# Performance work log

Measured on AMD Instinct MI355X. Metric: run time of the kernel, lower is better.

## Reference

```python
import jax, jax.numpy as jnp
import numpy as np

K = 2048      # codebook_size
D = 64        # codebook_dim
B = 32
T = 4096
W = 0.99      # codebook_loss_weight (EMA decay)
THRESH = 1.0  # discard_vec_threshold


def setup_inputs() -> dict:
    key = jax.random.key(0)
    k1, k2 = jax.random.split(key, 2)
    x = jax.random.normal(k1, (B, D, T), jnp.float32)
    codebook = jax.random.normal(k2, (K, D), jnp.float32)
    codebook_avg = codebook.copy()
    vector_usage = jnp.ones((K,), jnp.float32)
    perm = jnp.arange(B * T, dtype=jnp.int32)  # deterministic stand-in for randperm
    return dict(x=x, codebook=codebook, codebook_avg=codebook_avg,
                vector_usage=vector_usage, perm=perm)


def reference(x, codebook, codebook_avg, vector_usage, perm):
    Bv, E, Tv = x.shape
    sg = jax.lax.stop_gradient
    # preprocess: [B, E, T] -> [N, E]
    xf = jnp.transpose(x, (0, 2, 1)).reshape(-1, E)
    N = xf.shape[0]
    x_norm = jnp.linalg.norm(xf - jnp.mean(xf)) / np.sqrt(N * E)
    # squared euclidean distances [N, K]
    d = (jnp.sum(xf * xf, axis=-1, keepdims=True)
         - 2.0 * (xf @ codebook.T)
         + jnp.sum(codebook * codebook, axis=-1))
    idx = jnp.argmin(d, axis=-1)            # [N]
    fit = jnp.mean(jnp.min(d, axis=-1))
    q = codebook[idx]                       # [N, E] gather
    # --- update_codebook (torch.no_grad) ---
    cb_sum = jax.ops.segment_sum(sg(xf), idx, num_segments=K)          # onehot @ x
    counts = jax.ops.segment_sum(jnp.ones((N,), xf.dtype), idx, num_segments=K)
    new_avg = W * sg(codebook_avg) + (1.0 - W) * cb_sum
    new_usage = W * sg(vector_usage) + (1.0 - W) * counts
    keep = (new_usage >= THRESH).astype(xf.dtype)[:, None]
    random_shift = sg(xf)[perm][:K]
    new_codebook = keep * (new_avg / new_usage[:, None]) + (1.0 - keep) * random_shift
    vector_prob = counts / jnp.sum(counts)
    entropy = -jnp.sum(vector_prob * jnp.log(vector_prob + 1e-8))
    codebook_diff = jnp.linalg.norm(new_codebook - sg(codebook)) / np.sqrt(K * E)
    # --- commitment loss + straight-through ---
    commit_loss = jnp.sum((sg(q) - xf) ** 2) / (N * E)
    out = xf + sg(q - xf)
    out = jnp.transpose(out.reshape(Bv, Tv, E), (0, 2, 1))  # [B, E, T]
    return (out, commit_loss, fit, x_norm, new_codebook, new_avg, new_usage,
            entropy, codebook_diff)
```

## Files before the change

kernel.cpp:

```cpp
#include <hip/hip_runtime.h>
#include <math.h>

#define OUT_X      0
#define OUT_COMMIT 8388608
#define OUT_FIT    8388609
#define OUT_XNORM  8388610
#define OUT_NCB    8388611
#define OUT_NAVG   (8388611 + 131072)
#define OUT_NUSE   (8388611 + 262144)
#define OUT_ENT    (8388611 + 264192)
#define OUT_CBDIFF (8388611 + 264193)

#define WS_DACC    0
#define WS_COUNTS  64
#define WS_CBSUM   8256
#define WS_CURS    532544
#define WS_XN2     540736
#define WS_IDX     1065024
#define WS_CN2H    1589312
#define WS_SORTED  1597504
#define WS_CHI     2121792
#define WS_CLO     2383936
#define WS_ZERO_BYTES 532544

#define LO_SCALE5  32.0f

typedef _Float16 f16x8_t __attribute__((ext_vector_type(8)));
typedef float f32x16_t __attribute__((ext_vector_type(16)));

__device__ __forceinline__ void gload_lds16(const _Float16* g, _Float16* l) {
    __builtin_amdgcn_global_load_lds(
        (const __attribute__((address_space(1))) unsigned int*)(g),
        (__attribute__((address_space(3))) unsigned int*)(l), 16, 0, 0);
}

__global__ __launch_bounds__(256) void kern_prep_x(
    const float* __restrict__ x, float* __restrict__ xt,
    float* __restrict__ xn2, double* __restrict__ dacc)
{
    __shared__ __align__(16) float Xs[64][128];
    __shared__ float tmpA[4], tmpB[4];
    const int tid = threadIdx.x;
    const int n0 = blockIdx.x * 128;
    const int b = n0 >> 12, t0 = n0 & 4095;
    const float* xb = x + ((size_t)b << 18) + t0;
#pragma unroll
    for (int i = 0; i < 8; ++i) {
        int c = i * 256 + tid;
        int e = c >> 5, v4 = c & 31;
        float4 f = *(const float4*)(xb + ((size_t)e << 12) + (v4 << 2));
        *(float4*)&Xs[e][v4 << 2] = f;
    }
    __syncthreads();
    const int q = tid & 3, r0 = tid >> 2;
    float s1t = 0.f, s2t = 0.f;
#pragma unroll
    for (int h = 0; h < 2; ++h) {
        int r = r0 + (h << 6);
        float s2 = 0.f;
#pragma unroll
        for (int j = 0; j < 4; ++j) {
            int e = q * 16 + j * 4;
            float4 f = make_float4(Xs[e][r], Xs[e + 1][r], Xs[e + 2][r], Xs[e + 3][r]);
            *(float4*)(xt + (((size_t)(n0 + r)) << 6) + e) = f;
            s1t += f.x + f.y + f.z + f.w;
            s2 += f.x * f.x + f.y * f.y + f.z * f.z + f.w * f.w;
        }
        s2t += s2;
        float s2q = s2 + __shfl_xor(s2, 1, 64);
        s2q += __shfl_xor(s2q, 2, 64);
        if (q == 0) xn2[n0 + r] = s2q;
    }
    float rs = s1t, r2 = s2t;
#pragma unroll
    for (int m = 32; m >= 1; m >>= 1) {
        rs += __shfl_xor(rs, m, 64);
        r2 += __shfl_xor(r2, m, 64);
    }
    if ((tid & 63) == 0) { tmpA[tid >> 6] = rs; tmpB[tid >> 6] = r2; }
    __syncthreads();
    if (tid == 0) {
        atomicAdd(&dacc[0], (double)(tmpA[0] + tmpA[1] + tmpA[2] + tmpA[3]));
        atomicAdd(&dacc[1], (double)(tmpB[0] + tmpB[1] + tmpB[2] + tmpB[3]));
    }
}

__global__ __launch_bounds__(256) void kern_prep_cb(
    const float* __restrict__ cb, _Float16* __restrict__ chi,
    _Float16* __restrict__ clo, float* __restrict__ cn2h)
{
    __shared__ float Cs[128][68];
    const int tid = threadIdx.x;
    const int c0 = blockIdx.x * 128;
#pragma unroll
    for (int i = 0; i < 8; ++i) {
        int li = i * 256 + tid;
        int code = li >> 4, d4 = li & 15;
        float4 f = *(const float4*)(cb + (((size_t)(c0 + code)) << 6) + (d4 << 2));
        Cs[code][d4 * 4 + 0] = f.x; Cs[code][d4 * 4 + 1] = f.y;
        Cs[code][d4 * 4 + 2] = f.z; Cs[code][d4 * 4 + 3] = f.w;
    }
    __syncthreads();
    const int w = tid >> 6, lane = tid & 63;
    const int cl = (w << 5) + (lane & 31);
    const int g = lane >> 5;
    const int ktg = blockIdx.x * 4 + w;
#pragma unroll
    for (int s = 0; s < 4; ++s) {
        f16x8_t hh, ll;
#pragma unroll
        for (int i = 0; i < 8; ++i) {
            int k = 16 * s + 4 * g + (i & 3) + 8 * (i >> 2);
            float v = Cs[cl][k];
            _Float16 h = (_Float16)v;
            hh[i] = h;
            ll[i] = (_Float16)((v - (float)h) * LO_SCALE5);
        }
        *(f16x8_t*)(chi + (((size_t)(ktg * 4 + s)) << 9) + lane * 8) = hh;
        *(f16x8_t*)(clo + (((size_t)(ktg * 4 + s)) << 9) + lane * 8) = ll;
    }
    if (tid < 128) {
        float s = 0.f;
#pragma unroll
        for (int k = 0; k < 64; ++k) { float v = Cs[tid][k]; s = fmaf(v, v, s); }
        cn2h[c0 + tid] = -0.5f * s;
    }
}

__global__ __launch_bounds__(256, 2) void kern_argmin_mfma(
    const float* __restrict__ xt, const float* __restrict__ cn2h,
    const _Float16* __restrict__ chi, const _Float16* __restrict__ clo,
    const float* __restrict__ xn2, int* __restrict__ idxb,
    unsigned* __restrict__ counts, double* __restrict__ dacc)
{
    __shared__ __align__(16) _Float16 Bs[3][2][8][512];
    __shared__ float cvs[2048];
    const int tid = threadIdx.x;
    const int w = tid >> 6, lane = tid & 63;
    const int n0 = blockIdx.x * 256 + w * 64;
    const int l31 = lane & 31, g = lane >> 5;

    for (int i = tid; i < 2048; i += 256) cvs[i] = cn2h[i];

    f16x8_t ahi[2][4], alo5[2][4];
#pragma unroll
    for (int rb = 0; rb < 2; ++rb) {
        const float* xr = xt + ((size_t)(n0 + rb * 32 + l31) << 6) + 4 * g;
#pragma unroll
        for (int s = 0; s < 4; ++s) {
            float4 p = *(const float4*)(xr + 16 * s);
            float4 q = *(const float4*)(xr + 16 * s + 8);
            float vals[8] = {p.x, p.y, p.z, p.w, q.x, q.y, q.z, q.w};
#pragma unroll
            for (int i = 0; i < 8; ++i) {
                _Float16 h = (_Float16)vals[i];
                ahi[rb][s][i] = h;
                alo5[rb][s][i] = (_Float16)((vals[i] - (float)h) * LO_SCALE5);
            }
        }
    }
    float bestm[2][16]; int besti[2][16];
#pragma unroll
    for (int rb = 0; rb < 2; ++rb)
#pragma unroll
        for (int r = 0; r < 16; ++r) { bestm[rb][r] = -INFINITY; besti[rb][r] = 0; }

    __syncthreads();

#pragma unroll
    for (int kt = 0; kt < 2; ++kt)
#pragma unroll
        for (int j = 0; j < 4; ++j) {
            int seg = (j << 2) | w;
            int tt = seg >> 3, sh = seg & 7;
            const _Float16* src = ((sh & 1) ? clo : chi)
                + ((((size_t)(kt * 2 + tt)) * 4 + (sh >> 1)) << 9) + lane * 8;
            gload_lds16(src, &Bs[kt][tt][sh][0]);
        }

    int cur = 0, nxt = 2;
    for (int kt = 0; kt < 32; ++kt) {
        if (kt < 30) asm volatile("s_waitcnt vmcnt(4)" ::: "memory");
        else         asm volatile("s_waitcnt vmcnt(0)" ::: "memory");
        __builtin_amdgcn_s_barrier();
        if (kt + 2 < 32) {
#pragma unroll
            for (int j = 0; j < 4; ++j) {
                int seg = (j << 2) | w;
                int tt = seg >> 3, sh = seg & 7;
                const _Float16* src = ((sh & 1) ? clo : chi)
                    + ((((size_t)((kt + 2) * 2 + tt)) * 4 + (sh >> 1)) << 9) + lane * 8;
                gload_lds16(src, &Bs[nxt][tt][sh][0]);
            }
        }
#pragma unroll
        for (int tt = 0; tt < 2; ++tt) {
            const int tg = kt * 2 + tt;
            f16x8_t bh[4], bl[4];
#pragma unroll
            for (int s = 0; s < 4; ++s) {
                bh[s] = *(const f16x8_t*)&Bs[cur][tt][s * 2 + 0][lane * 8];
                bl[s] = *(const f16x8_t*)&Bs[cur][tt][s * 2 + 1][lane * 8];
            }
            float cv = cvs[(tg << 5) + l31];
            f32x16_t a0, a1;
#pragma unroll
            for (int r = 0; r < 16; ++r) { a0[r] = cv; a1[r] = cv; }
#pragma unroll
            for (int s = 0; s < 4; ++s) {
                a0 = __builtin_amdgcn_mfma_f32_32x32x16_f16(ahi[0][s], bh[s], a0, 0, 0, 0);
                a1 = __builtin_amdgcn_mfma_f32_32x32x16_f16(ahi[1][s], bh[s], a1, 0, 0, 0);
                f16x8_t bh5 = bh[s] * (_Float16)0.03125f;
                a0 = __builtin_amdgcn_mfma_f32_32x32x16_f16(alo5[0][s], bh5, a0, 0, 0, 0);
                a1 = __builtin_amdgcn_mfma_f32_32x32x16_f16(alo5[1][s], bh5, a1, 0, 0, 0);
                f16x8_t h50 = ahi[0][s] * (_Float16)0.03125f;
                f16x8_t h51 = ahi[1][s] * (_Float16)0.03125f;
                a0 = __builtin_amdgcn_mfma_f32_32x32x16_f16(h50, bl[s], a0, 0, 0, 0);
                a1 = __builtin_amdgcn_mfma_f32_32x32x16_f16(h51, bl[s], a1, 0, 0, 0);
            }
#pragma unroll
            for (int r = 0; r < 16; ++r) {
                if (a0[r] > bestm[0][r]) { bestm[0][r] = a0[r]; besti[0][r] = tg; }
                if (a1[r] > bestm[1][r]) { bestm[1][r] = a1[r]; besti[1][r] = tg; }
            }
        }
        cur = (cur == 2) ? 0 : cur + 1;
        nxt = (nxt == 2) ? 0 : nxt + 1;
    }
    float fs = 0.f;
#pragma unroll
    for (int rb = 0; rb < 2; ++rb)
#pragma unroll
        for (int r = 0; r < 16; ++r) {
            float mv = bestm[rb][r]; int mi = (besti[rb][r] << 5) + l31;
#pragma unroll
            for (int m = 1; m < 32; m <<= 1) {
                float ov = __shfl_xor(mv, m, 64);
                int oi = __shfl_xor(mi, m, 64);
                if (ov > mv || (ov == mv && oi < mi)) { mv = ov; mi = oi; }
            }
            if (l31 == 0) {
                int row = (r & 3) + 8 * (r >> 2) + 4 * g;
                int n = n0 + rb * 32 + row;
                idxb[n] = mi;
                atomicAdd(&counts[mi], 1u);
                fs += xn2[n] - 2.f * mv;
            }
        }
    if (l31 == 0) atomicAdd(&dacc[2], (double)fs);
}

__global__ void kern_scan(const unsigned* __restrict__ counts, unsigned* __restrict__ curs) {
    __shared__ unsigned wtot[4];
    const int tid = threadIdx.x;
    const int base = tid * 8;
    unsigned s[8]; unsigned tot = 0;
#pragma unroll
    for (int j = 0; j < 8; ++j) { s[j] = counts[base + j]; tot += s[j]; }
    unsigned v = tot;
    const int lane = tid & 63;
#pragma unroll
    for (int d = 1; d < 64; d <<= 1) {
        unsigned o = (unsigned)__shfl_up((int)v, d, 64);
        if (lane >= d) v += o;
    }
    if (lane == 63) wtot[tid >> 6] = v;
    __syncthreads();
    unsigned wbase = 0;
    for (int w = 0; w < (tid >> 6); ++w) wbase += wtot[w];
    unsigned run = wbase + v - tot;
#pragma unroll
    for (int j = 0; j < 8; ++j) { curs[base + j] = run; run += s[j]; }
}

__global__ void kern_scatter(const int* __restrict__ idxb, unsigned* __restrict__ curs,
                             unsigned* __restrict__ sorted) {
    const int n = blockIdx.x * 256 + threadIdx.x;
    int k = idxb[n];
    unsigned pos = atomicAdd(&curs[k], 1u);
    sorted[pos] = ((unsigned)k << 17) | (unsigned)n;
}

__global__ __launch_bounds__(256) void kern_chunk_reduce(
    const float* __restrict__ xt, const unsigned* __restrict__ sorted,
    float* __restrict__ cb_sum)
{
    const int tid = threadIdx.x;
    const int w = tid >> 6, lane = tid & 63;
    const int base = blockIdx.x * 256 + w * 64;
    int kcur = (int)(sorted[base] >> 17);
    float acc = 0.f;
#pragma unroll 4
    for (int it = 0; it < 16; ++it) {
        uint4 p = *(const uint4*)&sorted[base + it * 4];
        float v0 = xt[((size_t)(p.x & 0x1FFFFu) << 6) + lane];
        float v1 = xt[((size_t)(p.y & 0x1FFFFu) << 6) + lane];
        float v2 = xt[((size_t)(p.z & 0x1FFFFu) << 6) + lane];
        float v3 = xt[((size_t)(p.w & 0x1FFFFu) << 6) + lane];
        int k0 = (int)(p.x >> 17), k1 = (int)(p.y >> 17);
        int k2 = (int)(p.z >> 17), k3 = (int)(p.w >> 17);
        if (k0 != kcur) { atomicAdd(&cb_sum[(kcur << 6) + lane], acc); kcur = k0; acc = 0.f; }
        acc += v0;
        if (k1 != kcur) { atomicAdd(&cb_sum[(kcur << 6) + lane], acc); kcur = k1; acc = 0.f; }
        acc += v1;
        if (k2 != kcur) { atomicAdd(&cb_sum[(kcur << 6) + lane], acc); kcur = k2; acc = 0.f; }
        acc += v2;
        if (k3 != kcur) { atomicAdd(&cb_sum[(kcur << 6) + lane], acc); kcur = k3; acc = 0.f; }
        acc += v3;
    }
    atomicAdd(&cb_sum[(kcur << 6) + lane], acc);
}

__global__ __launch_bounds__(256) void kern_update(
    const float* __restrict__ cb_sum, const unsigned* __restrict__ counts,
    const float* __restrict__ cb, const float* __restrict__ cba,
    const float* __restrict__ usage, const int* __restrict__ perm,
    const float* __restrict__ xt, float* __restrict__ out,
    double* __restrict__ dacc)
{
    const int tid = threadIdx.x;
    const int i = blockIdx.x * 256 + tid;
    const int k = i >> 6, e = i & 63;
    float na = 0.99f * cba[i] + 0.01f * cb_sum[i];
    float nu = 0.99f * usage[k] + 0.01f * (float)counts[k];
    float ncb = (nu >= 1.0f) ? (na / nu)
                             : xt[((size_t)perm[k] << 6) + e];
    out[OUT_NAVG + i] = na;
    out[OUT_NCB + i] = ncb;
    if (e == 0) out[OUT_NUSE + k] = nu;
    float d = ncb - cb[i];
    float dd = d * d;
#pragma unroll
    for (int m = 32; m >= 1; m >>= 1) dd += __shfl_xor(dd, m, 64);
    if (e == 0) atomicAdd(&dacc[4], (double)dd);
}

__global__ __launch_bounds__(256) void kern_out(
    const float* __restrict__ x, const float* __restrict__ cb,
    const int* __restrict__ idxb, float* __restrict__ out,
    double* __restrict__ dacc) {
    __shared__ float tmp[4];
    const int tid = threadIdx.x;
    const int n0 = blockIdx.x * 256 + (tid & 63) * 4;
    const int ec = tid >> 6;
    const int b = n0 >> 12, t = n0 & 4095;
    int4 k4 = *(const int4*)(idxb + n0);
    const float* xb = x + ((size_t)b << 18) + t;
    float* ob = out + OUT_X + ((size_t)b << 18) + t;
    float cl = 0.f;
#pragma unroll
    for (int j = 0; j < 16; ++j) {
        int e = ec * 16 + j;
        float4 xv = *(const float4*)(xb + ((size_t)e << 12));
        float q0 = cb[((size_t)k4.x << 6) + e], q1 = cb[((size_t)k4.y << 6) + e];
        float q2 = cb[((size_t)k4.z << 6) + e], q3 = cb[((size_t)k4.w << 6) + e];
        float r0 = q0 - xv.x, r1 = q1 - xv.y, r2 = q2 - xv.z, r3 = q3 - xv.w;
        cl += r0 * r0 + r1 * r1 + r2 * r2 + r3 * r3;
        *(float4*)(ob + ((size_t)e << 12)) = make_float4(q0, q1, q2, q3);
    }
#pragma unroll
    for (int m = 32; m >= 1; m >>= 1) cl += __shfl_xor(cl, m, 64);
    if ((tid & 63) == 0) tmp[tid >> 6] = cl;
    __syncthreads();
    if (tid == 0) atomicAdd(&dacc[3], (double)(tmp[0] + tmp[1] + tmp[2] + tmp[3]));
}

__global__ void kern_scalars(const unsigned* __restrict__ counts,
                             const double* __restrict__ dacc, float* __restrict__ out) {
    __shared__ float tmp[4];
    __shared__ float totalSh;
    const int tid = threadIdx.x;
    float c = 0.f;
    for (int k = tid; k < 2048; k += 256) c += (float)counts[k];
#pragma unroll
    for (int m = 32; m >= 1; m >>= 1) c += __shfl_xor(c, m, 64);
    if ((tid & 63) == 0) tmp[tid >> 6] = c;
    __syncthreads();
    if (tid == 0) totalSh = tmp[0] + tmp[1] + tmp[2] + tmp[3];
    __syncthreads();
    const float total = totalSh;
    float ent = 0.f;
    for (int k = tid; k < 2048; k += 256) {
        float p = (float)counts[k] / total;
        ent -= p * logf(p + 1e-8f);
    }
#pragma unroll
    for (int m = 32; m >= 1; m >>= 1) ent += __shfl_xor(ent, m, 64);
    __syncthreads();
    if ((tid & 63) == 0) tmp[tid >> 6] = ent;
    __syncthreads();
    if (tid == 0) {
        float entropy = tmp[0] + tmp[1] + tmp[2] + tmp[3];
        out[OUT_COMMIT] = (float)(dacc[3] / 8388608.0);
        out[OUT_FIT]    = (float)(dacc[2] / 131072.0);
        double nd = 8388608.0;
        double var = dacc[1] - dacc[0] * dacc[0] / nd;
        if (var < 0.0) var = 0.0;
        out[OUT_XNORM] = (float)(sqrt(var) / sqrt(nd));
        out[OUT_ENT] = entropy;
        out[OUT_CBDIFF] = (float)(sqrt(dacc[4]) / sqrt(131072.0));
    }
}

extern "C" void kernel_launch(void* const* d_in, const int* in_sizes, int n_in,
                              void* d_out, int out_size, void* d_ws, size_t ws_size,
                              hipStream_t stream) {
    const float* x     = (const float*)d_in[0];
    const float* cb    = (const float*)d_in[1];
    const float* cba   = (const float*)d_in[2];
    const float* usage = (const float*)d_in[3];
    const int*   perm  = (const int*)d_in[4];
    float* out = (float*)d_out;
    char* ws = (char*)d_ws;
    double*    dacc   = (double*)(ws + WS_DACC);
    unsigned*  counts = (unsigned*)(ws + WS_COUNTS);
    float*     cbsum  = (float*)(ws + WS_CBSUM);
    unsigned*  curs   = (unsigned*)(ws + WS_CURS);
    float*     xn2    = (float*)(ws + WS_XN2);
    int*       idxb   = (int*)(ws + WS_IDX);
    float*     cn2h   = (float*)(ws + WS_CN2H);
    unsigned*  sorted = (unsigned*)(ws + WS_SORTED);
    _Float16*  chi    = (_Float16*)(ws + WS_CHI);
    _Float16*  clo    = (_Float16*)(ws + WS_CLO);
    float*     xt     = out + OUT_X;

    hipMemsetAsync(ws, 0, WS_ZERO_BYTES, stream);
    kern_prep_x<<<1024, 256, 0, stream>>>(x, xt, xn2, dacc);
    kern_prep_cb<<<16, 256, 0, stream>>>(cb, chi, clo, cn2h);
    kern_argmin_mfma<<<512, 256, 0, stream>>>(xt, cn2h, chi, clo, xn2, idxb, counts, dacc);
    kern_scan<<<1, 256, 0, stream>>>(counts, curs);
    kern_scatter<<<512, 256, 0, stream>>>(idxb, curs, sorted);
    kern_chunk_reduce<<<512, 256, 0, stream>>>(xt, sorted, cbsum);
    kern_update<<<512, 256, 0, stream>>>(cbsum, counts, cb, cba, usage, perm, xt, out, dacc);
    kern_out<<<512, 256, 0, stream>>>(x, cb, idxb, out, dacc);
    kern_scalars<<<1, 256, 0, stream>>>(counts, dacc, out);
}
```

Before: 276.4 us.

## Split codebook across blocks with atomicMax merge, fuse prep kernels, derive commit from fit

```diff
diff --git a/kernel.cpp b/kernel.cpp
--- a/kernel.cpp
+++ b/kernel.cpp
@@ -14,14 +14,15 @@
 #define WS_DACC    0
 #define WS_COUNTS  64
 #define WS_CBSUM   8256
-#define WS_CURS    532544
-#define WS_XN2     540736
-#define WS_IDX     1065024
-#define WS_CN2H    1589312
-#define WS_SORTED  1597504
-#define WS_CHI     2121792
-#define WS_CLO     2383936
-#define WS_ZERO_BYTES 532544
+#define WS_BEST    532544
+#define WS_CURS    1581120
+#define WS_XN2     1589312
+#define WS_IDX     2113600
+#define WS_CN2H    2637888
+#define WS_SORTED  2646080
+#define WS_CHI     3170368
+#define WS_CLO     3432512
+#define WS_ZERO_BYTES 1581120
 
 #define LO_SCALE5  32.0f
 
@@ -34,220 +35,232 @@
         (__attribute__((address_space(3))) unsigned int*)(l), 16, 0, 0);
 }
 
-__global__ __launch_bounds__(256) void kern_prep_x(
+__global__ __launch_bounds__(256) void kern_prep(
     const float* __restrict__ x, float* __restrict__ xt,
-    float* __restrict__ xn2, double* __restrict__ dacc)
-{
-    __shared__ __align__(16) float Xs[64][128];
-    __shared__ float tmpA[4], tmpB[4];
-    const int tid = threadIdx.x;
-    const int n0 = blockIdx.x * 128;
-    const int b = n0 >> 12, t0 = n0 & 4095;
-    const float* xb = x + ((size_t)b << 18) + t0;
-#pragma unroll
-    for (int i = 0; i < 8; ++i) {
-        int c = i * 256 + tid;
-        int e = c >> 5, v4 = c & 31;
-        float4 f = *(const float4*)(xb + ((size_t)e << 12) + (v4 << 2));
-        *(float4*)&Xs[e][v4 << 2] = f;
-    }
-    __syncthreads();
-    const int q = tid & 3, r0 = tid >> 2;
-    float s1t = 0.f, s2t = 0.f;
-#pragma unroll
-    for (int h = 0; h < 2; ++h) {
-        int r = r0 + (h << 6);
-        float s2 = 0.f;
-#pragma unroll
-        for (int j = 0; j < 4; ++j) {
-            int e = q * 16 + j * 4;
-            float4 f = make_float4(Xs[e][r], Xs[e + 1][r], Xs[e + 2][r], Xs[e + 3][r]);
-            *(float4*)(xt + (((size_t)(n0 + r)) << 6) + e) = f;
-            s1t += f.x + f.y + f.z + f.w;
-            s2 += f.x * f.x + f.y * f.y + f.z * f.z + f.w * f.w;
-        }
-        s2t += s2;
-        float s2q = s2 + __shfl_xor(s2, 1, 64);
-        s2q += __shfl_xor(s2q, 2, 64);
-        if (q == 0) xn2[n0 + r] = s2q;
-    }
-    float rs = s1t, r2 = s2t;
-#pragma unroll
-    for (int m = 32; m >= 1; m >>= 1) {
-        rs += __shfl_xor(rs, m, 64);
-        r2 += __shfl_xor(r2, m, 64);
-    }
-    if ((tid & 63) == 0) { tmpA[tid >> 6] = rs; tmpB[tid >> 6] = r2; }
-    __syncthreads();
-    if (tid == 0) {
-        atomicAdd(&dacc[0], (double)(tmpA[0] + tmpA[1] + tmpA[2] + tmpA[3]));
-        atomicAdd(&dacc[1], (double)(tmpB[0] + tmpB[1] + tmpB[2] + tmpB[3]));
-    }
-}
-
-__global__ __launch_bounds__(256) void kern_prep_cb(
+    float* __restrict__ xn2, double* __restrict__ dacc,
     const float* __restrict__ cb, _Float16* __restrict__ chi,
     _Float16* __restrict__ clo, float* __restrict__ cn2h)
 {
-    __shared__ float Cs[128][68];
-    const int tid = threadIdx.x;
-    const int c0 = blockIdx.x * 128;
-#pragma unroll
-    for (int i = 0; i < 8; ++i) {
-        int li = i * 256 + tid;
-        int code = li >> 4, d4 = li & 15;
-        float4 f = *(const float4*)(cb + (((size_t)(c0 + code)) << 6) + (d4 << 2));
-        Cs[code][d4 * 4 + 0] = f.x; Cs[code][d4 * 4 + 1] = f.y;
-        Cs[code][d4 * 4 + 2] = f.z; Cs[code][d4 * 4 + 3] = f.w;
-    }
-    __syncthreads();
-    const int w = tid >> 6, lane = tid & 63;
-    const int cl = (w << 5) + (lane & 31);
-    const int g = lane >> 5;
-    const int ktg = blockIdx.x * 4 + w;
-#pragma unroll
-    for (int s = 0; s < 4; ++s) {
-        f16x8_t hh, ll;
+    __shared__ __align__(16) char smem[128 * 68 * 4];
+    __shared__ float tmpA[4], tmpB[4];
+    const int tid = threadIdx.x;
+    if (blockIdx.x < 1024) {
+        float (*Xs)[128] = (float(*)[128])smem;
+        const int n0 = blockIdx.x * 128;
+        const int b = n0 >> 12, t0 = n0 & 4095;
+        const float* xb = x + ((size_t)b << 18) + t0;
 #pragma unroll
         for (int i = 0; i < 8; ++i) {
-            int k = 16 * s + 4 * g + (i & 3) + 8 * (i >> 2);
-            float v = Cs[cl][k];
-            _Float16 h = (_Float16)v;
-            hh[i] = h;
-            ll[i] = (_Float16)((v - (float)h) * LO_SCALE5);
-        }
-        *(f16x8_t*)(chi + (((size_t)(ktg * 4 + s)) << 9) + lane * 8) = hh;
-        *(f16x8_t*)(clo + (((size_t)(ktg * 4 + s)) << 9) + lane * 8) = ll;
-    }
-    if (tid < 128) {
-        float s = 0.f;
-#pragma unroll
-        for (int k = 0; k < 64; ++k) { float v = Cs[tid][k]; s = fmaf(v, v, s); }
-        cn2h[c0 + tid] = -0.5f * s;
-    }
-}
-
-__global__ __launch_bounds__(256, 2) void kern_argmin_mfma(
+            int c = i * 256 + tid;
+            int e = c >> 5, v4 = c & 31;
+            float4 f = *(const float4*)(xb + ((size_t)e << 12) + (v4 << 2));
+            *(float4*)&Xs[e][v4 << 2] = f;
+        }
+        __syncthreads();
+        const int q = tid & 3, r0 = tid >> 2;
+        float s1t = 0.f, s2t = 0.f;
+#pragma unroll
+        for (int h = 0; h < 2; ++h) {
+            int r = r0 + (h << 6);
+            float s2 = 0.f;
+#pragma unroll
+            for (int j = 0; j < 4; ++j) {
+                int e = q * 16 + j * 4;
+                float4 f = make_float4(Xs[e][r], Xs[e + 1][r], Xs[e + 2][r], Xs[e + 3][r]);
+                *(float4*)(xt + (((size_t)(n0 + r)) << 6) + e) = f;
+                s1t += f.x + f.y + f.z + f.w;
+                s2 += f.x * f.x + f.y * f.y + f.z * f.z + f.w * f.w;
+            }
+            s2t += s2;
+            float s2q = s2 + __shfl_xor(s2, 1, 64);
+            s2q += __shfl_xor(s2q, 2, 64);
+            if (q == 0) xn2[n0 + r] = s2q;
+        }
+        float rs = s1t, r2 = s2t;
+#pragma unroll
+        for (int m = 32; m >= 1; m >>= 1) {
+            rs += __shfl_xor(rs, m, 64);
+            r2 += __shfl_xor(r2, m, 64);
+        }
+        if ((tid & 63) == 0) { tmpA[tid >> 6] = rs; tmpB[tid >> 6] = r2; }
+        __syncthreads();
+        if (tid == 0) {
+            atomicAdd(&dacc[0], (double)(tmpA[0] + tmpA[1] + tmpA[2] + tmpA[3]));
+            atomicAdd(&dacc[1], (double)(tmpB[0] + tmpB[1] + tmpB[2] + tmpB[3]));
+        }
+    } else {
+        float (*Cs)[68] = (float(*)[68])smem;
+        const int c0 = (blockIdx.x - 1024) * 128;
+#pragma unroll
+        for (int i = 0; i < 8; ++i) {
+            int li = i * 256 + tid;
+            int code = li >> 4, d4 = li & 15;
+            float4 f = *(const float4*)(cb + (((size_t)(c0 + code)) << 6) + (d4 << 2));
+            Cs[code][d4 * 4 + 0] = f.x; Cs[code][d4 * 4 + 1] = f.y;
+            Cs[code][d4 * 4 + 2] = f.z; Cs[code][d4 * 4 + 3] = f.w;
+        }
+        __syncthreads();
+        const int w = tid >> 6, lane = tid & 63;
+        const int cl = (w << 5) + (lane & 31);
+        const int g = lane >> 5;
+        const int ktg = (blockIdx.x - 1024) * 4 + w;
+#pragma unroll
+        for (int s = 0; s < 4; ++s) {
+            f16x8_t hh, ll;
+#pragma unroll
+            for (int i = 0; i < 8; ++i) {
+                int k = 16 * s + 4 * g + (i & 3) + 8 * (i >> 2);
+                float v = Cs[cl][k];
+                _Float16 h = (_Float16)v;
+                hh[i] = h;
+                ll[i] = (_Float16)((v - (float)h) * LO_SCALE5);
+            }
+            *(f16x8_t*)(chi + (((size_t)(ktg * 4 + s)) << 9) + lane * 8) = hh;
+            *(f16x8_t*)(clo + (((size_t)(ktg * 4 + s)) << 9) + lane * 8) = ll;
+        }
+        if (tid < 128) {
+            float s = 0.f;
+#pragma unroll
+            for (int k = 0; k < 64; ++k) { float v = Cs[tid][k]; s = fmaf(v, v, s); }
+            cn2h[c0 + tid] = -0.5f * s;
+        }
+    }
+}
+
+__global__ __launch_bounds__(256) void kern_argmin_mfma(
     const float* __restrict__ xt, const float* __restrict__ cn2h,
     const _Float16* __restrict__ chi, const _Float16* __restrict__ clo,
-    const float* __restrict__ xn2, int* __restrict__ idxb,
-    unsigned* __restrict__ counts, double* __restrict__ dacc)
+    unsigned long long* __restrict__ bestbuf)
 {
-    __shared__ __align__(16) _Float16 Bs[3][2][8][512];
-    __shared__ float cvs[2048];
+    __shared__ __align__(16) _Float16 Bs[8][8][512];
     const int tid = threadIdx.x;
     const int w = tid >> 6, lane = tid & 63;
-    const int n0 = blockIdx.x * 256 + w * 64;
     const int l31 = lane & 31, g = lane >> 5;
-
-    for (int i = tid; i < 2048; i += 256) cvs[i] = cn2h[i];
-
-    f16x8_t ahi[2][4], alo5[2][4];
-#pragma unroll
-    for (int rb = 0; rb < 2; ++rb) {
-        const float* xr = xt + ((size_t)(n0 + rb * 32 + l31) << 6) + 4 * g;
-#pragma unroll
-        for (int s = 0; s < 4; ++s) {
-            float4 p = *(const float4*)(xr + 16 * s);
-            float4 q = *(const float4*)(xr + 16 * s + 8);
-            float vals[8] = {p.x, p.y, p.z, p.w, q.x, q.y, q.z, q.w};
-#pragma unroll
-            for (int i = 0; i < 8; ++i) {
-                _Float16 h = (_Float16)vals[i];
-                ahi[rb][s][i] = h;
-                alo5[rb][s][i] = (_Float16)((vals[i] - (float)h) * LO_SCALE5);
-            }
-        }
-    }
-    float bestm[2][16]; int besti[2][16];
-#pragma unroll
-    for (int rb = 0; rb < 2; ++rb)
-#pragma unroll
-        for (int r = 0; r < 16; ++r) { bestm[rb][r] = -INFINITY; besti[rb][r] = 0; }
-
-    __syncthreads();
-
-#pragma unroll
-    for (int kt = 0; kt < 2; ++kt)
-#pragma unroll
-        for (int j = 0; j < 4; ++j) {
-            int seg = (j << 2) | w;
-            int tt = seg >> 3, sh = seg & 7;
-            const _Float16* src = ((sh & 1) ? clo : chi)
-                + ((((size_t)(kt * 2 + tt)) * 4 + (sh >> 1)) << 9) + lane * 8;
-            gload_lds16(src, &Bs[kt][tt][sh][0]);
-        }
-
-    int cur = 0, nxt = 2;
-    for (int kt = 0; kt < 32; ++kt) {
-        if (kt < 30) asm volatile("s_waitcnt vmcnt(4)" ::: "memory");
-        else         asm volatile("s_waitcnt vmcnt(0)" ::: "memory");
-        __builtin_amdgcn_s_barrier();
-        if (kt + 2 < 32) {
-#pragma unroll
-            for (int j = 0; j < 4; ++j) {
-                int seg = (j << 2) | w;
-                int tt = seg >> 3, sh = seg & 7;
-                const _Float16* src = ((sh & 1) ? clo : chi)
-                    + ((((size_t)((kt + 2) * 2 + tt)) * 4 + (sh >> 1)) << 9) + lane * 8;
-                gload_lds16(src, &Bs[nxt][tt][sh][0]);
-            }
-        }
-#pragma unroll
-        for (int tt = 0; tt < 2; ++tt) {
-            const int tg = kt * 2 + tt;
+    const int oct = blockIdx.x & 7;
+    const int rg  = blockIdx.x >> 3;
+
+#pragma unroll
+    for (int j = 0; j < 16; ++j) {
+        int seg = (j << 2) | w;
+        int tt = seg >> 3, sh = seg & 7;
+        const _Float16* src = ((sh & 1) ? clo : chi)
+            + ((((size_t)(oct * 8 + tt)) * 4 + (sh >> 1)) << 9) + lane * 8;
+        gload_lds16(src, &Bs[tt][sh][0]);
+    }
+    __syncthreads();
+
+    for (int it = 0; it < 4; ++it) {
+        const int nw = rg * 1024 + it * 256 + w * 64;
+        f16x8_t ahi[2][4], alo5[2][4];
+#pragma unroll
+        for (int rb = 0; rb < 2; ++rb) {
+            const float* xr = xt + ((size_t)(nw + rb * 32 + l31) << 6) + 4 * g;
+#pragma unroll
+            for (int s = 0; s < 4; ++s) {
+                float4 p = *(const float4*)(xr + 16 * s);
+                float4 q = *(const float4*)(xr + 16 * s + 8);
+                float vals[8] = {p.x, p.y, p.z, p.w, q.x, q.y, q.z, q.w};
+#pragma unroll
+                for (int i = 0; i < 8; ++i) {
+                    _Float16 h = (_Float16)vals[i];
+                    ahi[rb][s][i] = h;
+                    alo5[rb][s][i] = (_Float16)((vals[i] - (float)h) * LO_SCALE5);
+                }
+            }
+        }
+        float bestm[2][16]; int besti[2][16];
+#pragma unroll
+        for (int rb = 0; rb < 2; ++rb)
+#pragma unroll
+            for (int r = 0; r < 16; ++r) { bestm[rb][r] = -INFINITY; besti[rb][r] = 0; }
+
+#pragma unroll
+        for (int tt = 0; tt < 8; ++tt) {
+            float cv = cn2h[(oct << 8) + (tt << 5) + l31];
             f16x8_t bh[4], bl[4];
 #pragma unroll
             for (int s = 0; s < 4; ++s) {
-                bh[s] = *(const f16x8_t*)&Bs[cur][tt][s * 2 + 0][lane * 8];
-                bl[s] = *(const f16x8_t*)&Bs[cur][tt][s * 2 + 1][lane * 8];
-            }
-            float cv = cvs[(tg << 5) + l31];
+                bh[s] = *(const f16x8_t*)&Bs[tt][s * 2 + 0][lane * 8];
+                bl[s] = *(const f16x8_t*)&Bs[tt][s * 2 + 1][lane * 8];
+            }
             f32x16_t a0, a1;
 #pragma unroll
-            for (int r = 0; r < 16; ++r) { a0[r] = cv; a1[r] = cv; }
+            for (int r = 0; r < 16; ++r) { a0[r] = 0.f; a1[r] = 0.f; }
+            __builtin_amdgcn_s_setprio(1);
+#pragma unroll
+            for (int s = 0; s < 4; ++s) {
+                a0 = __builtin_amdgcn_mfma_f32_32x32x16_f16(ahi[0][s], bl[s], a0, 0, 0, 0);
+                a1 = __builtin_amdgcn_mfma_f32_32x32x16_f16(ahi[1][s], bl[s], a1, 0, 0, 0);
+            }
+#pragma unroll
+            for (int s = 0; s < 4; ++s) {
+                a0 = __builtin_amdgcn_mfma_f32_32x32x16_f16(alo5[0][s], bh[s], a0, 0, 0, 0);
+                a1 = __builtin_amdgcn_mfma_f32_32x32x16_f16(alo5[1][s], bh[s], a1, 0, 0, 0);
+            }
+#pragma unroll
+            for (int r = 0; r < 16; ++r) {
+                a0[r] = fmaf(a0[r], 0.03125f, cv);
+                a1[r] = fmaf(a1[r], 0.03125f, cv);
+            }
 #pragma unroll
             for (int s = 0; s < 4; ++s) {
                 a0 = __builtin_amdgcn_mfma_f32_32x32x16_f16(ahi[0][s], bh[s], a0, 0, 0, 0);
                 a1 = __builtin_amdgcn_mfma_f32_32x32x16_f16(ahi[1][s], bh[s], a1, 0, 0, 0);
-                f16x8_t bh5 = bh[s] * (_Float16)0.03125f;
-                a0 = __builtin_amdgcn_mfma_f32_32x32x16_f16(alo5[0][s], bh5, a0, 0, 0, 0);
-                a1 = __builtin_amdgcn_mfma_f32_32x32x16_f16(alo5[1][s], bh5, a1, 0, 0, 0);
-                f16x8_t h50 = ahi[0][s] * (_Float16)0.03125f;
-                f16x8_t h51 = ahi[1][s] * (_Float16)0.03125f;
-                a0 = __builtin_amdgcn_mfma_f32_32x32x16_f16(h50, bl[s], a0, 0, 0, 0);
-                a1 = __builtin_amdgcn_mfma_f32_32x32x16_f16(h51, bl[s], a1, 0, 0, 0);
-            }
+            }
+            __builtin_amdgcn_s_setprio(0);
 #pragma unroll
             for (int r = 0; r < 16; ++r) {
-                if (a0[r] > bestm[0][r]) { bestm[0][r] = a0[r]; besti[0][r] = tg; }
-                if (a1[r] > bestm[1][r]) { bestm[1][r] = a1[r]; besti[1][r] = tg; }
-            }
-        }
-        cur = (cur == 2) ? 0 : cur + 1;
-        nxt = (nxt == 2) ? 0 : nxt + 1;
-    }
-    float fs = 0.f;
-#pragma unroll
-    for (int rb = 0; rb < 2; ++rb)
-#pragma unroll
-        for (int r = 0; r < 16; ++r) {
-            float mv = bestm[rb][r]; int mi = (besti[rb][r] << 5) + l31;
-#pragma unroll
-            for (int m = 1; m < 32; m <<= 1) {
-                float ov = __shfl_xor(mv, m, 64);
-                int oi = __shfl_xor(mi, m, 64);
-                if (ov > mv || (ov == mv && oi < mi)) { mv = ov; mi = oi; }
-            }
-            if (l31 == 0) {
-                int row = (r & 3) + 8 * (r >> 2) + 4 * g;
-                int n = n0 + rb * 32 + row;
-                idxb[n] = mi;
-                atomicAdd(&counts[mi], 1u);
-                fs += xn2[n] - 2.f * mv;
-            }
-        }
-    if (l31 == 0) atomicAdd(&dacc[2], (double)fs);
+                if (a0[r] > bestm[0][r]) { bestm[0][r] = a0[r]; besti[0][r] = tt; }
+                if (a1[r] > bestm[1][r]) { bestm[1][r] = a1[r]; besti[1][r] = tt; }
+            }
+        }
+#pragma unroll
+        for (int rb = 0; rb < 2; ++rb)
+#pragma unroll
+            for (int r = 0; r < 16; ++r) {
+                float mv = bestm[rb][r];
+                int mi = (besti[rb][r] << 5) + l31;
+#pragma unroll
+                for (int m = 1; m < 32; m <<= 1) {
+                    float ov = __shfl_xor(mv, m, 64);
+                    int oi = __shfl_xor(mi, m, 64);
+                    if (ov > mv || (ov == mv && oi < mi)) { mv = ov; mi = oi; }
+                }
+                if (l31 == 0) {
+                    int row = (r & 3) + 8 * (r >> 2) + 4 * g;
+                    int n = nw + rb * 32 + row;
+                    int gidx = (oct << 8) + mi;
+                    unsigned bits = __float_as_uint(mv);
+                    unsigned mono = bits ^ ((unsigned)((int)bits >> 31) | 0x80000000u);
+                    unsigned long long packed =
+                        ((unsigned long long)mono << 32) | (unsigned)(~gidx);
+                    atomicMax(bestbuf + n, packed);
+                }
+            }
+    }
+}
+
+__global__ __launch_bounds__(256) void kern_merge(
+    const unsigned long long* __restrict__ bestbuf, const float* __restrict__ xn2,
+    int* __restrict__ idxb, unsigned* __restrict__ counts,
+    double* __restrict__ dacc)
+{
+    __shared__ float tmp[4];
+    const int tid = threadIdx.x;
+    const int n = blockIdx.x * 256 + tid;
+    unsigned long long p = bestbuf[n];
+    unsigned mono = (unsigned)(p >> 32);
+    int gidx = (int)(~(unsigned)(p & 0xFFFFFFFFu));
+    unsigned bits = mono ^ ((mono >> 31) ? 0x80000000u : 0xFFFFFFFFu);
+    float mv = __uint_as_float(bits);
+    idxb[n] = gidx;
+    atomicAdd(&counts[gidx], 1u);
+    float fs = xn2[n] - 2.f * mv;
+#pragma unroll
+    for (int m = 32; m >= 1; m >>= 1) fs += __shfl_xor(fs, m, 64);
+    if ((tid & 63) == 0) tmp[tid >> 6] = fs;
+    __syncthreads();
+    if (tid == 0) atomicAdd(&dacc[2], (double)(tmp[0] + tmp[1] + tmp[2] + tmp[3]));
 }
 
 __global__ void kern_scan(const unsigned* __restrict__ counts, unsigned* __restrict__ curs) {
@@ -335,36 +348,6 @@
     if (e == 0) atomicAdd(&dacc[4], (double)dd);
 }
 
-__global__ __launch_bounds__(256) void kern_out(
-    const float* __restrict__ x, const float* __restrict__ cb,
-    const int* __restrict__ idxb, float* __restrict__ out,
-    double* __restrict__ dacc) {
-    __shared__ float tmp[4];
-    const int tid = threadIdx.x;
-    const int n0 = blockIdx.x * 256 + (tid & 63) * 4;
-    const int ec = tid >> 6;
-    const int b = n0 >> 12, t = n0 & 4095;
-    int4 k4 = *(const int4*)(idxb + n0);
-    const float* xb = x + ((size_t)b << 18) + t;
-    float* ob = out + OUT_X + ((size_t)b << 18) + t;
-    float cl = 0.f;
-#pragma unroll
-    for (int j = 0; j < 16; ++j) {
-        int e = ec * 16 + j;
-        float4 xv = *(const float4*)(xb + ((size_t)e << 12));
-        float q0 = cb[((size_t)k4.x << 6) + e], q1 = cb[((size_t)k4.y << 6) + e];
-        float q2 = cb[((size_t)k4.z << 6) + e], q3 = cb[((size_t)k4.w << 6) + e];
-        float r0 = q0 - xv.x, r1 = q1 - xv.y, r2 = q2 - xv.z, r3 = q3 - xv.w;
-        cl += r0 * r0 + r1 * r1 + r2 * r2 + r3 * r3;
-        *(float4*)(ob + ((size_t)e << 12)) = make_float4(q0, q1, q2, q3);
-    }
-#pragma unroll
-    for (int m = 32; m >= 1; m >>= 1) cl += __shfl_xor(cl, m, 64);
-    if ((tid & 63) == 0) tmp[tid >> 6] = cl;
-    __syncthreads();
-    if (tid == 0) atomicAdd(&dacc[3], (double)(tmp[0] + tmp[1] + tmp[2] + tmp[3]));
-}
-
 __global__ void kern_scalars(const unsigned* __restrict__ counts,
                              const double* __restrict__ dacc, float* __restrict__ out) {
     __shared__ float tmp[4];
@@ -391,7 +374,7 @@
     __syncthreads();
     if (tid == 0) {
         float entropy = tmp[0] + tmp[1] + tmp[2] + tmp[3];
-        out[OUT_COMMIT] = (float)(dacc[3] / 8388608.0);
+        out[OUT_COMMIT] = (float)(dacc[2] / 8388608.0);
         out[OUT_FIT]    = (float)(dacc[2] / 131072.0);
         double nd = 8388608.0;
         double var = dacc[1] - dacc[0] * dacc[0] / nd;
@@ -399,6 +382,24 @@
         out[OUT_XNORM] = (float)(sqrt(var) / sqrt(nd));
         out[OUT_ENT] = entropy;
         out[OUT_CBDIFF] = (float)(sqrt(dacc[4]) / sqrt(131072.0));
+    }
+}
+
+__global__ __launch_bounds__(256) void kern_out(
+    const float* __restrict__ cb, const int* __restrict__ idxb,
+    float* __restrict__ out) {
+    const int tid = threadIdx.x;
+    const int n0 = blockIdx.x * 256 + (tid & 63) * 4;
+    const int ec = tid >> 6;
+    const int b = n0 >> 12, t = n0 & 4095;
+    int4 k4 = *(const int4*)(idxb + n0);
+    float* ob = out + OUT_X + ((size_t)b << 18) + t;
+#pragma unroll
+    for (int j = 0; j < 16; ++j) {
+        int e = ec * 16 + j;
+        float q0 = cb[((size_t)k4.x << 6) + e], q1 = cb[((size_t)k4.y << 6) + e];
+        float q2 = cb[((size_t)k4.z << 6) + e], q3 = cb[((size_t)k4.w << 6) + e];
+        *(float4*)(ob + ((size_t)e << 12)) = make_float4(q0, q1, q2, q3);
     }
 }
 
@@ -412,26 +413,27 @@
     const int*   perm  = (const int*)d_in[4];
     float* out = (float*)d_out;
     char* ws = (char*)d_ws;
-    double*    dacc   = (double*)(ws + WS_DACC);
-    unsigned*  counts = (unsigned*)(ws + WS_COUNTS);
-    float*     cbsum  = (float*)(ws + WS_CBSUM);
-    unsigned*  curs   = (unsigned*)(ws + WS_CURS);
-    float*     xn2    = (float*)(ws + WS_XN2);
-    int*       idxb   = (int*)(ws + WS_IDX);
-    float*     cn2h   = (float*)(ws + WS_CN2H);
-    unsigned*  sorted = (unsigned*)(ws + WS_SORTED);
-    _Float16*  chi    = (_Float16*)(ws + WS_CHI);
-    _Float16*  clo    = (_Float16*)(ws + WS_CLO);
-    float*     xt     = out + OUT_X;
+    double*             dacc    = (double*)(ws + WS_DACC);
+    unsigned*           counts  = (unsigned*)(ws + WS_COUNTS);
+    float*              cbsum   = (float*)(ws + WS_CBSUM);
+    unsigned long long* bestbuf = (unsigned long long*)(ws + WS_BEST);
+    unsigned*           curs    = (unsigned*)(ws + WS_CURS);
+    float*              xn2     = (float*)(ws + WS_XN2);
+    int*                idxb    = (int*)(ws + WS_IDX);
+    float*              cn2h    = (float*)(ws + WS_CN2H);
+    unsigned*           sorted  = (unsigned*)(ws + WS_SORTED);
+    _Float16*           chi     = (_Float16*)(ws + WS_CHI);
+    _Float16*           clo     = (_Float16*)(ws + WS_CLO);
+    float*              xt      = out + OUT_X;
 
     hipMemsetAsync(ws, 0, WS_ZERO_BYTES, stream);
-    kern_prep_x<<<1024, 256, 0, stream>>>(x, xt, xn2, dacc);
-    kern_prep_cb<<<16, 256, 0, stream>>>(cb, chi, clo, cn2h);
-    kern_argmin_mfma<<<512, 256, 0, stream>>>(xt, cn2h, chi, clo, xn2, idxb, counts, dacc);
+    kern_prep<<<1040, 256, 0, stream>>>(x, xt, xn2, dacc, cb, chi, clo, cn2h);
+    kern_argmin_mfma<<<1024, 256, 0, stream>>>(xt, cn2h, chi, clo, bestbuf);
+    kern_merge<<<512, 256, 0, stream>>>(bestbuf, xn2, idxb, counts, dacc);
     kern_scan<<<1, 256, 0, stream>>>(counts, curs);
     kern_scatter<<<512, 256, 0, stream>>>(idxb, curs, sorted);
     kern_chunk_reduce<<<512, 256, 0, stream>>>(xt, sorted, cbsum);
     kern_update<<<512, 256, 0, stream>>>(cbsum, counts, cb, cba, usage, perm, xt, out, dacc);
-    kern_out<<<512, 256, 0, stream>>>(x, cb, idxb, out, dacc);
     kern_scalars<<<1, 256, 0, stream>>>(counts, dacc, out);
-}
+    kern_out<<<512, 256, 0, stream>>>(cb, idxb, out);
+}
```

Result: slower. 776.1 us (+180.8%).
